# Kernel tuning notes

Hardware: AMD Instinct MI355X
Metric: run time of the kernel (lower is better)

Reference implementation:

```python
import jax, jax.numpy as jnp
import numpy as np
import math

N = 4096
E = 512          # hidden_dim
H = 8            # num_heads
MAX_STEPS = 100
D_TIME = E // 2  # 256
D_STAT = E // 4  # 128


def _time_encoding():
    # sinusoidal table [MAX_STEPS, D_TIME], matching the torch buffer
    pos = jnp.arange(MAX_STEPS, dtype=jnp.float32)[:, None]
    div = jnp.exp(jnp.arange(0, D_TIME, 2, dtype=jnp.float32) * (-math.log(10000.0) / D_TIME))
    ang = pos * div  # [MAX_STEPS, D_TIME//2]
    return jnp.stack([jnp.sin(ang), jnp.cos(ang)], axis=-1).reshape(MAX_STEPS, D_TIME)


def setup_inputs() -> dict:
    key = jax.random.key(0)
    ks = jax.random.split(key, 12)
    w = 0.02
    return {
        "x": jax.random.normal(ks[0], (N, E), jnp.float32),
        "derived_mask": jax.random.randint(ks[1], (N,), 0, 2, jnp.int32),
        "step_numbers": jax.random.randint(ks[2], (N,), 0, MAX_STEPS, jnp.int32),
        "status_embed": jax.random.normal(ks[3], (2, D_STAT), jnp.float32),
        "in_proj_w": jax.random.normal(ks[4], (3 * E, E), jnp.float32) * w,
        "in_proj_b": jnp.zeros((3 * E,), jnp.float32),
        "out_proj_w": jax.random.normal(ks[5], (E, E), jnp.float32) * w,
        "out_proj_b": jnp.zeros((E,), jnp.float32),
        "mlp_w": jax.random.normal(ks[6], (E, E + D_STAT + D_TIME), jnp.float32) * w,
        "mlp_b": jnp.zeros((E,), jnp.float32),
        "ln_gamma": jnp.ones((E,), jnp.float32),
        "ln_beta": jnp.zeros((E,), jnp.float32),
    }


def reference(x, derived_mask, step_numbers, status_embed, in_proj_w, in_proj_b,
              out_proj_w, out_proj_b, mlp_w, mlp_b, ln_gamma, ln_beta):
    n = x.shape[0]
    hd = E // H

    # --- multihead self-attention with dynamic step-based mask ---
    qkv = x @ in_proj_w.T + in_proj_b                      # [N, 3E]
    q, k, v = jnp.split(qkv, 3, axis=-1)
    q = q.reshape(n, H, hd).transpose(1, 0, 2)             # [H, N, hd]
    k = k.reshape(n, H, hd).transpose(1, 0, 2)
    v = v.reshape(n, H, hd).transpose(1, 0, 2)

    scores = jnp.einsum('hnd,hmd->hnm', q, k) / math.sqrt(hd)   # [H, N, N]
    # mask[i, j] = True  <=>  step[j] - step[i] < 0 (blocked, -inf)
    blocked = (step_numbers[None, :] - step_numbers[:, None]) < 0
    scores = jnp.where(blocked[None, :, :], jnp.float32(-1e9), scores)
    attn = jax.nn.softmax(scores, axis=-1)
    ctx = jnp.einsum('hnm,hmd->hnd', attn, v)              # [H, N, hd]
    ctx = ctx.transpose(1, 0, 2).reshape(n, E)
    x_att = ctx @ out_proj_w.T + out_proj_b                # [N, E]

    # --- embeddings ---
    status = status_embed[derived_mask]                    # [N, E/4]
    step_c = jnp.clip(step_numbers, 0, MAX_STEPS - 1)
    time_emb = _time_encoding()[step_c]                    # [N, E/2]

    # --- fused output MLP: Linear -> LayerNorm -> ReLU ---
    combined = jnp.concatenate([x_att, status, time_emb], axis=-1)  # [N, 7E/4]
    h = combined @ mlp_w.T + mlp_b                         # [N, E]
    mu = jnp.mean(h, axis=-1, keepdims=True)
    var = jnp.mean((h - mu) ** 2, axis=-1, keepdims=True)
    h = (h - mu) / jnp.sqrt(var + 1e-5) * ln_gamma + ln_beta
    out = jnp.maximum(h, 0.0)
    return x + out
```

## Files before the change

kernel.cpp:

```cpp
#include <hip/hip_runtime.h>
#include <hip/hip_bf16.h>
#include <math.h>

typedef __bf16 bf16x8 __attribute__((ext_vector_type(8)));
typedef __bf16 bf16x4 __attribute__((ext_vector_type(4)));
typedef float f32x4 __attribute__((ext_vector_type(4)));

#define N_TOK 4096
#define EDIM 512
#define NHEAD 8
#define HD 64
#define LDCOMB 896
#define NBIN 100
#define SPLITK 8
#define BK 64

#define NU_CVT 3264
#define NU_TC 64
#define NU_ADD 128
#define NU_TMAT 128
#define NB_PREP (NU_CVT + NU_TC + NU_ADD + NU_TMAT + 1)

__global__ __launch_bounds__(256) void prep_kernel(
    const float* __restrict__ x, const float* __restrict__ w_in,
    const float* __restrict__ w_mlp, const float* __restrict__ w_out,
    const float* __restrict__ status, const float* __restrict__ out_b,
    const float* __restrict__ mlp_b, const int* __restrict__ steps,
    __bf16* __restrict__ x_bf, __bf16* __restrict__ wqkv_bf,
    __bf16* __restrict__ wmlp_bf, __bf16* __restrict__ woutT_bf,
    float* __restrict__ add2, __bf16* __restrict__ tmat,
    int* __restrict__ perm, int* __restrict__ sstep,
    int* __restrict__ bs_row, int* __restrict__ qinfo) {
    __shared__ float T[64][65];
    __shared__ int hist[NBIN];
    __shared__ int offs[NBIN];
    const int bid = blockIdx.x;
    const int tid = threadIdx.x;
    const int wave = tid >> 6, lane = tid & 63;

    if (bid < NU_CVT) {
        int i = bid * 256 + tid;
        const int n0 = N_TOK * EDIM / 4;
        const int n1 = 3 * EDIM * EDIM / 4;
        const float* src; __bf16* dst;
        if (i < n0)           { src = x; dst = x_bf; }
        else if (i < n0 + n1) { i -= n0; src = w_in; dst = wqkv_bf; }
        else                  { i -= n0 + n1; src = w_mlp; dst = wmlp_bf; }
        const float4 v = ((const float4*)src)[i];
        bf16x4 o;
        o[0] = (__bf16)v.x; o[1] = (__bf16)v.y; o[2] = (__bf16)v.z; o[3] = (__bf16)v.w;
        ((bf16x4*)dst)[i] = o;
    } else if (bid < NU_CVT + NU_TC) {
        const int b2 = bid - NU_CVT;
        const int m0 = (b2 >> 3) * 64, k0 = (b2 & 7) * 64;
        const int row = tid >> 2, c4 = (tid & 3) * 16;
        #pragma unroll
        for (int i = 0; i < 4; i++) {
            const float4 v = *(const float4*)&w_out[(size_t)(m0 + row) * EDIM + k0 + c4 + i * 4];
            T[row][c4 + i * 4 + 0] = v.x;
            T[row][c4 + i * 4 + 1] = v.y;
            T[row][c4 + i * 4 + 2] = v.z;
            T[row][c4 + i * 4 + 3] = v.w;
        }
        __syncthreads();
        const int kr = tid >> 2, m16 = (tid & 3) * 16;
        bf16x8 o0, o1;
        #pragma unroll
        for (int i = 0; i < 8; i++) o0[i] = (__bf16)T[m16 + i][kr];
        #pragma unroll
        for (int i = 0; i < 8; i++) o1[i] = (__bf16)T[m16 + 8 + i][kr];
        *(bf16x8*)&woutT_bf[(size_t)(k0 + kr) * EDIM + m0 + m16] = o0;
        *(bf16x8*)&woutT_bf[(size_t)(k0 + kr) * EDIM + m0 + m16 + 8] = o1;
    } else if (bid < NU_CVT + NU_TC + NU_ADD) {
        const int j = (bid - NU_CVT - NU_TC) * 4 + wave;
        const float* wr = w_mlp + (size_t)j * LDCOMB;
        const int k8 = lane * 8;
        const float4 wa = *(const float4*)&wr[k8], wb = *(const float4*)&wr[k8 + 4];
        const float4 oa = *(const float4*)&out_b[k8], ob = *(const float4*)&out_b[k8 + 4];
        float b = wa.x * oa.x + wa.y * oa.y + wa.z * oa.z + wa.w * oa.w +
                  wb.x * ob.x + wb.y * ob.y + wb.z * ob.z + wb.w * ob.w;
        const int c2 = lane * 2;
        const float w0 = wr[EDIM + c2], w1 = wr[EDIM + c2 + 1];
        float s0 = status[c2] * w0 + status[c2 + 1] * w1;
        float s1 = status[128 + c2] * w0 + status[129 + c2] * w1;
        #pragma unroll
        for (int m = 1; m < 64; m <<= 1) {
            b += __shfl_xor(b, m);
            s0 += __shfl_xor(s0, m);
            s1 += __shfl_xor(s1, m);
        }
        if (lane == 0) {
            const float bb = b + mlp_b[j];
            add2[j] = s0 + bb;
            add2[EDIM + j] = s1 + bb;
        }
    } else if (bid < NU_CVT + NU_TC + NU_ADD + NU_TMAT) {
        const int st = bid - NU_CVT - NU_TC - NU_ADD;
        const int c = tid;
        const int pp = c >> 1;
        const float div = expf((float)(2 * pp) * (-9.210340371976184f / 256.0f));
        const float ang = (float)st * div;
        tmat[st * 256 + c] = (__bf16)((c & 1) ? cosf(ang) : sinf(ang));
    } else {
        if (tid < NBIN) hist[tid] = 0;
        __syncthreads();
        for (int i = tid; i < N_TOK; i += 256)
            atomicAdd(&hist[min(max(steps[i], 0), NBIN - 1)], 1);
        __syncthreads();
        if (tid == 0) {
            int acc = 0;
            for (int s = 0; s < NBIN; s++) { offs[s] = acc; acc += hist[s]; }
        }
        __syncthreads();
        if (tid < NBIN) hist[tid] = offs[tid];
        __syncthreads();
        for (int i = tid; i < N_TOK; i += 256) {
            const int s = min(max(steps[i], 0), NBIN - 1);
            const int pos = atomicAdd(&offs[s], 1);
            perm[pos] = i;
            sstep[pos] = s;
        }
        __syncthreads();
        for (int q = tid; q < N_TOK; q += 256)
            bs_row[q] = hist[sstep[q]];
        __syncthreads();
        for (int qt = tid; qt < 64; qt += 256) {
            qinfo[qt * 2] = bs_row[qt * 64] & ~(BK - 1);
            qinfo[qt * 2 + 1] = bs_row[qt * 64 + 63];
        }
    }
}

__global__ __launch_bounds__(256) void gemm2_kernel(const __bf16* __restrict__ x_bf,
                                                    const __bf16* __restrict__ wqkv_bf,
                                                    const float* __restrict__ b_in,
                                                    const int* __restrict__ perm,
                                                    __bf16* __restrict__ qs,
                                                    __bf16* __restrict__ ks,
                                                    __bf16* __restrict__ vt,
                                                    const __bf16* __restrict__ wmlp_bf,
                                                    const __bf16* __restrict__ woutT_bf,
                                                    __bf16* __restrict__ weff_bf,
                                                    const __bf16* __restrict__ tmat,
                                                    float* __restrict__ tv) {
    __shared__ __attribute__((aligned(16))) union {
        struct { __bf16 As[128][40]; __bf16 Bs[128][40]; } g;
        __bf16 T[128][72];
    } sm;
    __shared__ int pr[128];
    const int bid = blockIdx.x;
    const int tid = threadIdx.x;
    const int wave = tid >> 6, lane = tid & 63;
    const int wm = (wave >> 1) * 64, wn = (wave & 1) * 64;
    const int lr = lane & 15, lq = lane >> 4;

    const __bf16 *A, *B;
    int lda, ldb, bm, bn, K, mode;
    if (bid < 384) {
        A = x_bf; lda = EDIM; B = wqkv_bf; ldb = EDIM; K = EDIM; mode = 0;
        bm = (bid & 31) * 128; bn = (bid >> 5) * 128;
        if (tid < 128) pr[tid] = perm[bm + tid];
    } else if (bid < 400) {
        const int b2 = bid - 384;
        A = wmlp_bf; lda = LDCOMB; B = woutT_bf; ldb = EDIM; K = EDIM; mode = 1;
        bm = (b2 & 3) * 128; bn = (b2 >> 2) * 128;
    } else {
        const int b3 = bid - 400;
        A = tmat; lda = 256; B = wmlp_bf + 640; ldb = LDCOMB; K = 256; mode = 2;
        bm = 0; bn = b3 * 128;
    }

    f32x4 acc[4][4] = {};
    for (int k0 = 0; k0 < K; k0 += 32) {
        __syncthreads();
        #pragma unroll
        for (int c = tid; c < 512; c += 256) {
            const int row = c >> 2, k8 = (c & 3) * 8;
            const int arow = (mode == 0) ? pr[row] : (bm + row);
            *(bf16x8*)&sm.g.As[row][k8] = *(const bf16x8*)&A[(size_t)arow * lda + k0 + k8];
            *(bf16x8*)&sm.g.Bs[row][k8] = *(const bf16x8*)&B[(size_t)(bn + row) * ldb + k0 + k8];
        }
        __syncthreads();
        bf16x8 af[4], bfr[4];
        #pragma unroll
        for (int i = 0; i < 4; i++) {
            af[i]  = *(const bf16x8*)&sm.g.As[wm + i * 16 + lr][lq * 8];
            bfr[i] = *(const bf16x8*)&sm.g.Bs[wn + i * 16 + lr][lq * 8];
        }
        #pragma unroll
        for (int i = 0; i < 4; i++)
            #pragma unroll
            for (int j = 0; j < 4; j++)
                acc[i][j] = __builtin_amdgcn_mfma_f32_16x16x32_bf16(af[i], bfr[j], acc[i][j], 0, 0, 0);
    }

    if (mode == 1) {
        #pragma unroll
        for (int i = 0; i < 4; i++)
            #pragma unroll
            for (int j = 0; j < 4; j++) {
                const int col = bn + wn + j * 16 + lr;
                #pragma unroll
                for (int r = 0; r < 4; r++)
                    weff_bf[(size_t)(bm + wm + i * 16 + lq * 4 + r) * EDIM + col] =
                        (__bf16)acc[i][j][r];
            }
    } else if (mode == 2) {
        #pragma unroll
        for (int i = 0; i < 4; i++)
            #pragma unroll
            for (int j = 0; j < 4; j++) {
                const int col = bn + wn + j * 16 + lr;
                #pragma unroll
                for (int r = 0; r < 4; r++) {
                    const int row = wm + i * 16 + lq * 4 + r;
                    if (row < NBIN) tv[(size_t)row * EDIM + col] = acc[i][j][r];
                }
            }
    } else if (bn < 512) {
        const float SC = 0.125f * 1.44269504f;
        #pragma unroll
        for (int i = 0; i < 4; i++)
            #pragma unroll
            for (int j = 0; j < 4; j++) {
                const int col = bn + wn + j * 16 + lr;
                const float bv = b_in[col];
                #pragma unroll
                for (int r = 0; r < 4; r++)
                    qs[(size_t)(bm + wm + i * 16 + lq * 4 + r) * EDIM + col] =
                        (__bf16)((acc[i][j][r] + bv) * SC);
            }
    } else if (bn < 1024) {
        #pragma unroll
        for (int i = 0; i < 4; i++)
            #pragma unroll
            for (int j = 0; j < 4; j++) {
                const int col = bn + wn + j * 16 + lr;
                const float bv = b_in[col];
                #pragma unroll
                for (int r = 0; r < 4; r++)
                    ks[(size_t)(bm + wm + i * 16 + lq * 4 + r) * EDIM + (col - 512)] =
                        (__bf16)(acc[i][j][r] + bv);
            }
    } else {
        #pragma unroll
        for (int half = 0; half < 2; half++) {
            __syncthreads();
            if ((wave & 1) == half) {
                #pragma unroll
                for (int i = 0; i < 4; i++)
                    #pragma unroll
                    for (int j = 0; j < 4; j++) {
                        const float bv = b_in[bn + wn + j * 16 + lr];
                        #pragma unroll
                        for (int r = 0; r < 4; r++)
                            sm.T[wm + i * 16 + lq * 4 + r][j * 16 + lr] =
                                (__bf16)(acc[i][j][r] + bv);
                    }
            }
            __syncthreads();
            for (int u = tid; u < 1024; u += 256) {
                const int d = u & 63, t8 = (u >> 6) * 8;
                bf16x8 v;
                #pragma unroll
                for (int j = 0; j < 8; j++) v[j] = sm.T[t8 + j][d];
                const int dim = (bn - 1024) + half * 64 + d;
                *(bf16x8*)&vt[(size_t)dim * N_TOK + bm + t8] = v;
            }
        }
    }
}

__global__ __launch_bounds__(256) void attn_kernel(const __bf16* __restrict__ qs,
                                                   const __bf16* __restrict__ ks,
                                                   const __bf16* __restrict__ vt,
                                                   const int* __restrict__ bs_row,
                                                   const int* __restrict__ qinfo,
                                                   __bf16* __restrict__ po,
                                                   float* __restrict__ pl) {
    __shared__ __attribute__((aligned(16))) __bf16 Ks[BK][72];
    __shared__ __attribute__((aligned(16))) __bf16 Vs[64][BK + 8];
    __shared__ __attribute__((aligned(16))) __bf16 Ps[64][BK + 8];

    const int h = blockIdx.y;
    const int qtile = blockIdx.x;
    const int ck = blockIdx.z;
    const int tid = threadIdx.x, wave = tid >> 6, lane = tid & 63;
    const int lr = lane & 15, lq = lane >> 4;
    const int qbase = qtile * 64 + wave * 16;

    const int kt0 = qinfo[qtile * 2];
    const int bs_blockmax = qinfo[qtile * 2 + 1];
    const int nt = (N_TOK - kt0) / BK;
    const int kta = kt0 + ((nt * ck) / SPLITK) * BK;
    const int ktb = kt0 + ((nt * (ck + 1)) / SPLITK) * BK;

    bf16x8 aq[2];
    {
        const __bf16* qrow = qs + (size_t)(qbase + lr) * EDIM + h * HD;
        aq[0] = *(const bf16x8*)&qrow[lq * 8];
        aq[1] = *(const bf16x8*)&qrow[32 + lq * 8];
    }
    int bs_r[4];
    #pragma unroll
    for (int r = 0; r < 4; r++) bs_r[r] = bs_row[qbase + lq * 4 + r];

    float l_i[4] = {0.f, 0.f, 0.f, 0.f};
    f32x4 o[4] = {};

    const __bf16* kbase = ks + h * HD;
    const __bf16* vbase = vt + (size_t)h * HD * N_TOK;

    const int r0 = tid >> 3, r1 = r0 + 32, k8 = (tid & 7) * 8;
    bf16x8 kr0, kr1, vr0, vr1;
    if (kta < ktb) {
        kr0 = *(const bf16x8*)&kbase[(size_t)(kta + r0) * EDIM + k8];
        kr1 = *(const bf16x8*)&kbase[(size_t)(kta + r1) * EDIM + k8];
        vr0 = *(const bf16x8*)&vbase[(size_t)r0 * N_TOK + kta + k8];
        vr1 = *(const bf16x8*)&vbase[(size_t)r1 * N_TOK + kta + k8];
    }

    for (int kt = kta; kt < ktb; kt += BK) {
        __syncthreads();
        *(bf16x8*)&Ks[r0][k8] = kr0;
        *(bf16x8*)&Ks[r1][k8] = kr1;
        *(bf16x8*)&Vs[r0][k8] = vr0;
        *(bf16x8*)&Vs[r1][k8] = vr1;
        __syncthreads();
        if (kt + BK < ktb) {
            kr0 = *(const bf16x8*)&kbase[(size_t)(kt + BK + r0) * EDIM + k8];
            kr1 = *(const bf16x8*)&kbase[(size_t)(kt + BK + r1) * EDIM + k8];
            vr0 = *(const bf16x8*)&vbase[(size_t)r0 * N_TOK + kt + BK + k8];
            vr1 = *(const bf16x8*)&vbase[(size_t)r1 * N_TOK + kt + BK + k8];
        }

        f32x4 s[4];
        #pragma unroll
        for (int t = 0; t < 4; t++) {
            bf16x8 b0 = *(const bf16x8*)&Ks[t * 16 + lr][lq * 8];
            bf16x8 b1 = *(const bf16x8*)&Ks[t * 16 + lr][32 + lq * 8];
            f32x4 a = {};
            a = __builtin_amdgcn_mfma_f32_16x16x32_bf16(aq[0], b0, a, 0, 0, 0);
            a = __builtin_amdgcn_mfma_f32_16x16x32_bf16(aq[1], b1, a, 0, 0, 0);
            s[t] = a;
        }
        if (kt < bs_blockmax) {
            #pragma unroll
            for (int t = 0; t < 4; t++) {
                const int col = kt + t * 16 + lr;
                #pragma unroll
                for (int r = 0; r < 4; r++)
                    if (col < bs_r[r]) s[t][r] = -1e9f;
            }
        }
        #pragma unroll
        for (int t = 0; t < 4; t++) {
            #pragma unroll
            for (int r = 0; r < 4; r++) {
                const float pr = exp2f(s[t][r]);
                l_i[r] += pr;
                Ps[wave * 16 + lq * 4 + r][t * 16 + lr] = (__bf16)pr;
            }
        }
        #pragma unroll
        for (int ks2 = 0; ks2 < 2; ks2++) {
            bf16x8 ap = *(const bf16x8*)&Ps[wave * 16 + lr][ks2 * 32 + lq * 8];
            #pragma unroll
            for (int dt = 0; dt < 4; dt++) {
                bf16x8 bv = *(const bf16x8*)&Vs[dt * 16 + lr][ks2 * 32 + lq * 8];
                o[dt] = __builtin_amdgcn_mfma_f32_16x16x32_bf16(ap, bv, o[dt], 0, 0, 0);
            }
        }
    }

    #pragma unroll
    for (int r = 0; r < 4; r++) {
        float v = l_i[r];
        v += __shfl_xor(v, 1);
        v += __shfl_xor(v, 2);
        v += __shfl_xor(v, 4);
        v += __shfl_xor(v, 8);
        l_i[r] = v;
    }
    __bf16* pob = po + (((size_t)(ck * NHEAD + h) * N_TOK) + qbase) * HD;
    #pragma unroll
    for (int dt = 0; dt < 4; dt++)
        #pragma unroll
        for (int r = 0; r < 4; r++)
            pob[(lq * 4 + r) * HD + dt * 16 + lr] = (__bf16)o[dt][r];
    if (lr == 0) {
        #pragma unroll
        for (int r = 0; r < 4; r++)
            pl[(size_t)(ck * NHEAD + h) * N_TOK + qbase + lq * 4 + r] = l_i[r];
    }
}

__global__ __launch_bounds__(256) void combine_kernel(const __bf16* __restrict__ po,
                                                      const float* __restrict__ pl,
                                                      const int* __restrict__ perm,
                                                      __bf16* __restrict__ ctx) {
    const int e = blockIdx.x * 256 + threadIdx.x;
    const int q = e >> 7;
    const int col = (e & 127) * 4;
    const int h = col >> 6, d = col & 63;
    float s0 = 0.f, s1 = 0.f, s2 = 0.f, s3 = 0.f, l = 0.f;
    #pragma unroll
    for (int c = 0; c < SPLITK; c++) {
        const bf16x4 v = *(const bf16x4*)&po[(((size_t)(c * NHEAD + h) * N_TOK) + q) * HD + d];
        s0 += (float)v[0]; s1 += (float)v[1]; s2 += (float)v[2]; s3 += (float)v[3];
        l += pl[(size_t)(c * NHEAD + h) * N_TOK + q];
    }
    const float rl = 1.0f / l;
    bf16x4 o;
    o[0] = (__bf16)(s0 * rl); o[1] = (__bf16)(s1 * rl);
    o[2] = (__bf16)(s2 * rl); o[3] = (__bf16)(s3 * rl);
    *(bf16x4*)&ctx[(size_t)perm[q] * EDIM + col] = o;
}

__global__ __launch_bounds__(256) void gemm_fused(const __bf16* __restrict__ A,
                                                  const __bf16* __restrict__ B,
                                                  const int* __restrict__ dmask,
                                                  const int* __restrict__ steps,
                                                  const float* __restrict__ add2,
                                                  const float* __restrict__ tv,
                                                  float* __restrict__ C) {
    __shared__ __attribute__((aligned(16))) __bf16 As[128][40];
    __shared__ __attribute__((aligned(16))) __bf16 Bs[128][40];
    const int tid = threadIdx.x;
    const int wave = tid >> 6, lane = tid & 63;
    const int wm = (wave >> 1) * 64, wn = (wave & 1) * 64;
    const int bm = blockIdx.x * 128, bn = blockIdx.y * 128;
    const int lr = lane & 15, lq = lane >> 4;

    f32x4 acc[4][4] = {};
    for (int k0 = 0; k0 < EDIM; k0 += 32) {
        __syncthreads();
        #pragma unroll
        for (int c = tid; c < 512; c += 256) {
            const int row = c >> 2, k8 = (c & 3) * 8;
            *(bf16x8*)&As[row][k8] = *(const bf16x8*)&A[(size_t)(bm + row) * EDIM + k0 + k8];
            *(bf16x8*)&Bs[row][k8] = *(const bf16x8*)&B[(size_t)(bn + row) * EDIM + k0 + k8];
        }
        __syncthreads();
        bf16x8 af[4], bfr[4];
        #pragma unroll
        for (int i = 0; i < 4; i++) {
            af[i]  = *(const bf16x8*)&As[wm + i * 16 + lr][lq * 8];
            bfr[i] = *(const bf16x8*)&Bs[wn + i * 16 + lr][lq * 8];
        }
        #pragma unroll
        for (int i = 0; i < 4; i++)
            #pragma unroll
            for (int j = 0; j < 4; j++)
                acc[i][j] = __builtin_amdgcn_mfma_f32_16x16x32_bf16(af[i], bfr[j], acc[i][j], 0, 0, 0);
    }

    int dmr[4][4], str[4][4];
    #pragma unroll
    for (int i = 0; i < 4; i++)
        #pragma unroll
        for (int r = 0; r < 4; r++) {
            const int row = bm + wm + i * 16 + lq * 4 + r;
            dmr[i][r] = dmask[row];
            str[i][r] = min(max(steps[row], 0), NBIN - 1);
        }
    #pragma unroll
    for (int i = 0; i < 4; i++)
        #pragma unroll
        for (int j = 0; j < 4; j++) {
            const int col = bn + wn + j * 16 + lr;
            #pragma unroll
            for (int r = 0; r < 4; r++) {
                const int row = bm + wm + i * 16 + lq * 4 + r;
                C[(size_t)row * EDIM + col] = acc[i][j][r]
                    + add2[dmr[i][r] * EDIM + col] + tv[str[i][r] * EDIM + col];
            }
        }
}

__global__ __launch_bounds__(256) void ln_kernel(const float* __restrict__ h,
                                                 const float* __restrict__ x,
                                                 const float* __restrict__ gamma,
                                                 const float* __restrict__ beta,
                                                 float* __restrict__ out) {
    const int row = blockIdx.x * 4 + (threadIdx.x >> 6);
    const int lane = threadIdx.x & 63;
    const float* hr = h + (size_t)row * EDIM;
    float4 v0 = ((const float4*)hr)[lane];
    float4 v1 = ((const float4*)hr)[64 + lane];
    float sum = v0.x + v0.y + v0.z + v0.w + v1.x + v1.y + v1.z + v1.w;
    float sq = v0.x * v0.x + v0.y * v0.y + v0.z * v0.z + v0.w * v0.w +
               v1.x * v1.x + v1.y * v1.y + v1.z * v1.z + v1.w * v1.w;
    #pragma unroll
    for (int m = 1; m < 64; m <<= 1) {
        sum += __shfl_xor(sum, m);
        sq  += __shfl_xor(sq, m);
    }
    const float mean = sum * (1.0f / EDIM);
    const float var = sq * (1.0f / EDIM) - mean * mean;
    const float rstd = rsqrtf(var + 1e-5f);
    const float* xr = x + (size_t)row * EDIM;
    float* orow = out + (size_t)row * EDIM;
    #pragma unroll
    for (int half = 0; half < 2; half++) {
        const float4 v = half ? v1 : v0;
        const int cb = half * 256 + lane * 4;
        const float* vp = (const float*)&v;
        float4 res;
        float tmp[4];
        #pragma unroll
        for (int i = 0; i < 4; i++) {
            const int c = cb + i;
            float t = (vp[i] - mean) * rstd * gamma[c] + beta[c];
            t = fmaxf(t, 0.f);
            tmp[i] = xr[c] + t;
        }
        res.x = tmp[0]; res.y = tmp[1]; res.z = tmp[2]; res.w = tmp[3];
        ((float4*)orow)[cb >> 2] = res;
    }
}

extern "C" void kernel_launch(void* const* d_in, const int* in_sizes, int n_in,
                              void* d_out, int out_size, void* d_ws, size_t ws_size,
                              hipStream_t stream) {
    const float* x      = (const float*)d_in[0];
    const int*   dmask  = (const int*)d_in[1];
    const int*   steps  = (const int*)d_in[2];
    const float* status = (const float*)d_in[3];
    const float* w_in   = (const float*)d_in[4];
    const float* b_in   = (const float*)d_in[5];
    const float* w_out  = (const float*)d_in[6];
    const float* b_out  = (const float*)d_in[7];
    const float* w_mlp  = (const float*)d_in[8];
    const float* b_mlp  = (const float*)d_in[9];
    const float* gamma  = (const float*)d_in[10];
    const float* beta   = (const float*)d_in[11];
    float* out = (float*)d_out;

    char* ws = (char*)d_ws;
    size_t off = 0;
    auto alloc = [&](size_t bytes) {
        void* ptr = ws + off;
        off = (off + bytes + 255) & ~(size_t)255;
        return ptr;
    };
    __bf16* x_bf    = (__bf16*)alloc((size_t)N_TOK * EDIM * 2);
    __bf16* wqkv_bf = (__bf16*)alloc((size_t)3 * EDIM * EDIM * 2);
    __bf16* wmlp_bf = (__bf16*)alloc((size_t)EDIM * LDCOMB * 2);
    __bf16* woutT_bf= (__bf16*)alloc((size_t)EDIM * EDIM * 2);
    __bf16* weff_bf = (__bf16*)alloc((size_t)EDIM * EDIM * 2);
    __bf16* qs_bf   = (__bf16*)alloc((size_t)N_TOK * EDIM * 2);
    __bf16* ks_bf   = (__bf16*)alloc((size_t)N_TOK * EDIM * 2);
    __bf16* vt_bf   = (__bf16*)alloc((size_t)EDIM * N_TOK * 2);
    __bf16* ctx_bf  = (__bf16*)alloc((size_t)N_TOK * EDIM * 2);
    float*  h_f32   = (float*)alloc((size_t)N_TOK * EDIM * 4);
    int*    perm    = (int*)alloc(N_TOK * 4);
    int*    sstep   = (int*)alloc(N_TOK * 4);
    int*    bs_row  = (int*)alloc(N_TOK * 4);
    int*    qinfo   = (int*)alloc(128 * 4);
    __bf16* po      = (__bf16*)alloc((size_t)SPLITK * NHEAD * N_TOK * HD * 2);
    float*  pl      = (float*)alloc((size_t)SPLITK * NHEAD * N_TOK * 4);
    float*  add2    = (float*)alloc(2 * EDIM * 4);
    float*  tv      = (float*)alloc((size_t)NBIN * EDIM * 4);
    __bf16* tmat    = (__bf16*)alloc(128 * 256 * 2);

    prep_kernel<<<NB_PREP, 256, 0, stream>>>(
        x, w_in, w_mlp, w_out, status, b_out, b_mlp, steps,
        x_bf, wqkv_bf, wmlp_bf, woutT_bf, add2, tmat, perm, sstep, bs_row, qinfo);
    gemm2_kernel<<<404, 256, 0, stream>>>(
        x_bf, wqkv_bf, b_in, perm, qs_bf, ks_bf, vt_bf,
        wmlp_bf, woutT_bf, weff_bf, tmat, tv);
    attn_kernel<<<dim3(64, NHEAD, SPLITK), 256, 0, stream>>>(
        qs_bf, ks_bf, vt_bf, bs_row, qinfo, po, pl);
    combine_kernel<<<(N_TOK * EDIM) / 1024, 256, 0, stream>>>(po, pl, perm, ctx_bf);
    gemm_fused<<<dim3(N_TOK / 128, EDIM / 128), 256, 0, stream>>>(
        ctx_bf, weff_bf, dmask, steps, add2, tv, h_f32);
    ln_kernel<<<N_TOK / 4, 256, 0, stream>>>(h_f32, x, gamma, beta, out);
}
```

Baseline: 204.2 us.

## Fuse fp32-to-bf16 conversion into GEMM tile loads and narrow final GEMM tiles

Drops the separate conversion pass over x, w_in and w_mlp from the prep kernel. The QKV and weight GEMMs now read fp32 directly and convert to bf16 while loading tiles into shared memory, which removes a full write-and-reread of the bf16 copies. In exchange those GEMM loads fetch twice as many bytes per element and take a runtime branch on the source type. Separately, the final fused GEMM switches from 128x128 to 128x64 tiles, doubling the block count to 256 so more of the GPU is occupied, at the cost of reloading A tiles more often.

```diff
diff --git a/kernel.cpp b/kernel.cpp
--- a/kernel.cpp
+++ b/kernel.cpp
@@ -15,19 +15,25 @@
 #define SPLITK 8
 #define BK 64
 
-#define NU_CVT 3264
 #define NU_TC 64
 #define NU_ADD 128
 #define NU_TMAT 128
-#define NB_PREP (NU_CVT + NU_TC + NU_ADD + NU_TMAT + 1)
+#define NB_PREP (NU_TC + NU_ADD + NU_TMAT + 1)
+
+__device__ __forceinline__ bf16x8 cvt8(const float* p) {
+    const float4 a = *(const float4*)p;
+    const float4 b = *(const float4*)(p + 4);
+    bf16x8 o;
+    o[0] = (__bf16)a.x; o[1] = (__bf16)a.y; o[2] = (__bf16)a.z; o[3] = (__bf16)a.w;
+    o[4] = (__bf16)b.x; o[5] = (__bf16)b.y; o[6] = (__bf16)b.z; o[7] = (__bf16)b.w;
+    return o;
+}
 
 __global__ __launch_bounds__(256) void prep_kernel(
-    const float* __restrict__ x, const float* __restrict__ w_in,
     const float* __restrict__ w_mlp, const float* __restrict__ w_out,
     const float* __restrict__ status, const float* __restrict__ out_b,
     const float* __restrict__ mlp_b, const int* __restrict__ steps,
-    __bf16* __restrict__ x_bf, __bf16* __restrict__ wqkv_bf,
-    __bf16* __restrict__ wmlp_bf, __bf16* __restrict__ woutT_bf,
+    __bf16* __restrict__ woutT_bf,
     float* __restrict__ add2, __bf16* __restrict__ tmat,
     int* __restrict__ perm, int* __restrict__ sstep,
     int* __restrict__ bs_row, int* __restrict__ qinfo) {
@@ -38,21 +44,8 @@
     const int tid = threadIdx.x;
     const int wave = tid >> 6, lane = tid & 63;
 
-    if (bid < NU_CVT) {
-        int i = bid * 256 + tid;
-        const int n0 = N_TOK * EDIM / 4;
-        const int n1 = 3 * EDIM * EDIM / 4;
-        const float* src; __bf16* dst;
-        if (i < n0)           { src = x; dst = x_bf; }
-        else if (i < n0 + n1) { i -= n0; src = w_in; dst = wqkv_bf; }
-        else                  { i -= n0 + n1; src = w_mlp; dst = wmlp_bf; }
-        const float4 v = ((const float4*)src)[i];
-        bf16x4 o;
-        o[0] = (__bf16)v.x; o[1] = (__bf16)v.y; o[2] = (__bf16)v.z; o[3] = (__bf16)v.w;
-        ((bf16x4*)dst)[i] = o;
-    } else if (bid < NU_CVT + NU_TC) {
-        const int b2 = bid - NU_CVT;
-        const int m0 = (b2 >> 3) * 64, k0 = (b2 & 7) * 64;
+    if (bid < NU_TC) {
+        const int m0 = (bid >> 3) * 64, k0 = (bid & 7) * 64;
         const int row = tid >> 2, c4 = (tid & 3) * 16;
         #pragma unroll
         for (int i = 0; i < 4; i++) {
@@ -71,8 +64,8 @@
         for (int i = 0; i < 8; i++) o1[i] = (__bf16)T[m16 + 8 + i][kr];
         *(bf16x8*)&woutT_bf[(size_t)(k0 + kr) * EDIM + m0 + m16] = o0;
         *(bf16x8*)&woutT_bf[(size_t)(k0 + kr) * EDIM + m0 + m16 + 8] = o1;
-    } else if (bid < NU_CVT + NU_TC + NU_ADD) {
-        const int j = (bid - NU_CVT - NU_TC) * 4 + wave;
+    } else if (bid < NU_TC + NU_ADD) {
+        const int j = (bid - NU_TC) * 4 + wave;
         const float* wr = w_mlp + (size_t)j * LDCOMB;
         const int k8 = lane * 8;
         const float4 wa = *(const float4*)&wr[k8], wb = *(const float4*)&wr[k8 + 4];
@@ -94,8 +87,8 @@
             add2[j] = s0 + bb;
             add2[EDIM + j] = s1 + bb;
         }
-    } else if (bid < NU_CVT + NU_TC + NU_ADD + NU_TMAT) {
-        const int st = bid - NU_CVT - NU_TC - NU_ADD;
+    } else if (bid < NU_TC + NU_ADD + NU_TMAT) {
+        const int st = bid - NU_TC - NU_ADD;
         const int c = tid;
         const int pp = c >> 1;
         const float div = expf((float)(2 * pp) * (-9.210340371976184f / 256.0f));
@@ -131,14 +124,14 @@
     }
 }
 
-__global__ __launch_bounds__(256) void gemm2_kernel(const __bf16* __restrict__ x_bf,
-                                                    const __bf16* __restrict__ wqkv_bf,
+__global__ __launch_bounds__(256) void gemm2_kernel(const float* __restrict__ x,
+                                                    const float* __restrict__ w_in,
                                                     const float* __restrict__ b_in,
                                                     const int* __restrict__ perm,
                                                     __bf16* __restrict__ qs,
                                                     __bf16* __restrict__ ks,
                                                     __bf16* __restrict__ vt,
-                                                    const __bf16* __restrict__ wmlp_bf,
+                                                    const float* __restrict__ w_mlp,
                                                     const __bf16* __restrict__ woutT_bf,
                                                     __bf16* __restrict__ weff_bf,
                                                     const __bf16* __restrict__ tmat,
@@ -154,19 +147,20 @@
     const int wm = (wave >> 1) * 64, wn = (wave & 1) * 64;
     const int lr = lane & 15, lq = lane >> 4;
 
-    const __bf16 *A, *B;
+    const float *Af = nullptr, *Bf = nullptr;
+    const __bf16 *Ab = nullptr, *Bb = nullptr;
     int lda, ldb, bm, bn, K, mode;
     if (bid < 384) {
-        A = x_bf; lda = EDIM; B = wqkv_bf; ldb = EDIM; K = EDIM; mode = 0;
+        Af = x; lda = EDIM; Bf = w_in; ldb = EDIM; K = EDIM; mode = 0;
         bm = (bid & 31) * 128; bn = (bid >> 5) * 128;
         if (tid < 128) pr[tid] = perm[bm + tid];
     } else if (bid < 400) {
         const int b2 = bid - 384;
-        A = wmlp_bf; lda = LDCOMB; B = woutT_bf; ldb = EDIM; K = EDIM; mode = 1;
+        Af = w_mlp; lda = LDCOMB; Bb = woutT_bf; ldb = EDIM; K = EDIM; mode = 1;
         bm = (b2 & 3) * 128; bn = (b2 >> 2) * 128;
     } else {
         const int b3 = bid - 400;
-        A = tmat; lda = 256; B = wmlp_bf + 640; ldb = LDCOMB; K = 256; mode = 2;
+        Ab = tmat; lda = 256; Bf = w_mlp + 640; ldb = LDCOMB; K = 256; mode = 2;
         bm = 0; bn = b3 * 128;
     }
 
@@ -177,8 +171,13 @@
         for (int c = tid; c < 512; c += 256) {
             const int row = c >> 2, k8 = (c & 3) * 8;
             const int arow = (mode == 0) ? pr[row] : (bm + row);
-            *(bf16x8*)&sm.g.As[row][k8] = *(const bf16x8*)&A[(size_t)arow * lda + k0 + k8];
-            *(bf16x8*)&sm.g.Bs[row][k8] = *(const bf16x8*)&B[(size_t)(bn + row) * ldb + k0 + k8];
+            bf16x8 av, bv;
+            if (Af) av = cvt8(&Af[(size_t)arow * lda + k0 + k8]);
+            else    av = *(const bf16x8*)&Ab[(size_t)arow * lda + k0 + k8];
+            if (Bf) bv = cvt8(&Bf[(size_t)(bn + row) * ldb + k0 + k8]);
+            else    bv = *(const bf16x8*)&Bb[(size_t)(bn + row) * ldb + k0 + k8];
+            *(bf16x8*)&sm.g.As[row][k8] = av;
+            *(bf16x8*)&sm.g.Bs[row][k8] = bv;
         }
         __syncthreads();
         bf16x8 af[4], bfr[4];
@@ -425,39 +424,45 @@
                                                   const float* __restrict__ tv,
                                                   float* __restrict__ C) {
     __shared__ __attribute__((aligned(16))) __bf16 As[128][40];
-    __shared__ __attribute__((aligned(16))) __bf16 Bs[128][40];
+    __shared__ __attribute__((aligned(16))) __bf16 Bs[64][40];
     const int tid = threadIdx.x;
     const int wave = tid >> 6, lane = tid & 63;
-    const int wm = (wave >> 1) * 64, wn = (wave & 1) * 64;
-    const int bm = blockIdx.x * 128, bn = blockIdx.y * 128;
+    const int wm = wave * 32;
+    const int bm = blockIdx.x * 128, bn = blockIdx.y * 64;
     const int lr = lane & 15, lq = lane >> 4;
 
-    f32x4 acc[4][4] = {};
+    f32x4 acc[2][4] = {};
     for (int k0 = 0; k0 < EDIM; k0 += 32) {
         __syncthreads();
         #pragma unroll
-        for (int c = tid; c < 512; c += 256) {
-            const int row = c >> 2, k8 = (c & 3) * 8;
-            *(bf16x8*)&As[row][k8] = *(const bf16x8*)&A[(size_t)(bm + row) * EDIM + k0 + k8];
-            *(bf16x8*)&Bs[row][k8] = *(const bf16x8*)&B[(size_t)(bn + row) * EDIM + k0 + k8];
-        }
-        __syncthreads();
-        bf16x8 af[4], bfr[4];
-        #pragma unroll
-        for (int i = 0; i < 4; i++) {
-            af[i]  = *(const bf16x8*)&As[wm + i * 16 + lr][lq * 8];
-            bfr[i] = *(const bf16x8*)&Bs[wn + i * 16 + lr][lq * 8];
-        }
-        #pragma unroll
-        for (int i = 0; i < 4; i++)
+        for (int c = tid; c < 768; c += 256) {
+            if (c < 512) {
+                const int row = c >> 2, k8 = (c & 3) * 8;
+                *(bf16x8*)&As[row][k8] = *(const bf16x8*)&A[(size_t)(bm + row) * EDIM + k0 + k8];
+            } else {
+                const int c2 = c - 512;
+                const int row = c2 >> 2, k8 = (c2 & 3) * 8;
+                *(bf16x8*)&Bs[row][k8] = *(const bf16x8*)&B[(size_t)(bn + row) * EDIM + k0 + k8];
+            }
+        }
+        __syncthreads();
+        bf16x8 af[2], bfr[4];
+        #pragma unroll
+        for (int i = 0; i < 2; i++)
+            af[i] = *(const bf16x8*)&As[wm + i * 16 + lr][lq * 8];
+        #pragma unroll
+        for (int j = 0; j < 4; j++)
+            bfr[j] = *(const bf16x8*)&Bs[j * 16 + lr][lq * 8];
+        #pragma unroll
+        for (int i = 0; i < 2; i++)
             #pragma unroll
             for (int j = 0; j < 4; j++)
                 acc[i][j] = __builtin_amdgcn_mfma_f32_16x16x32_bf16(af[i], bfr[j], acc[i][j], 0, 0, 0);
     }
 
-    int dmr[4][4], str[4][4];
-    #pragma unroll
-    for (int i = 0; i < 4; i++)
+    int dmr[2][4], str[2][4];
+    #pragma unroll
+    for (int i = 0; i < 2; i++)
         #pragma unroll
         for (int r = 0; r < 4; r++) {
             const int row = bm + wm + i * 16 + lq * 4 + r;
@@ -465,10 +470,10 @@
             str[i][r] = min(max(steps[row], 0), NBIN - 1);
         }
     #pragma unroll
-    for (int i = 0; i < 4; i++)
+    for (int i = 0; i < 2; i++)
         #pragma unroll
         for (int j = 0; j < 4; j++) {
-            const int col = bn + wn + j * 16 + lr;
+            const int col = bn + j * 16 + lr;
             #pragma unroll
             for (int r = 0; r < 4; r++) {
                 const int row = bm + wm + i * 16 + lq * 4 + r;
@@ -544,9 +549,6 @@
         off = (off + bytes + 255) & ~(size_t)255;
         return ptr;
     };
-    __bf16* x_bf    = (__bf16*)alloc((size_t)N_TOK * EDIM * 2);
-    __bf16* wqkv_bf = (__bf16*)alloc((size_t)3 * EDIM * EDIM * 2);
-    __bf16* wmlp_bf = (__bf16*)alloc((size_t)EDIM * LDCOMB * 2);
     __bf16* woutT_bf= (__bf16*)alloc((size_t)EDIM * EDIM * 2);
     __bf16* weff_bf = (__bf16*)alloc((size_t)EDIM * EDIM * 2);
     __bf16* qs_bf   = (__bf16*)alloc((size_t)N_TOK * EDIM * 2);
@@ -565,15 +567,15 @@
     __bf16* tmat    = (__bf16*)alloc(128 * 256 * 2);
 
     prep_kernel<<<NB_PREP, 256, 0, stream>>>(
-        x, w_in, w_mlp, w_out, status, b_out, b_mlp, steps,
-        x_bf, wqkv_bf, wmlp_bf, woutT_bf, add2, tmat, perm, sstep, bs_row, qinfo);
+        w_mlp, w_out, status, b_out, b_mlp, steps,
+        woutT_bf, add2, tmat, perm, sstep, bs_row, qinfo);
     gemm2_kernel<<<404, 256, 0, stream>>>(
-        x_bf, wqkv_bf, b_in, perm, qs_bf, ks_bf, vt_bf,
-        wmlp_bf, woutT_bf, weff_bf, tmat, tv);
+        x, w_in, b_in, perm, qs_bf, ks_bf, vt_bf,
+        w_mlp, woutT_bf, weff_bf, tmat, tv);
     attn_kernel<<<dim3(64, NHEAD, SPLITK), 256, 0, stream>>>(
         qs_bf, ks_bf, vt_bf, bs_row, qinfo, po, pl);
     combine_kernel<<<(N_TOK * EDIM) / 1024, 256, 0, stream>>>(po, pl, perm, ctx_bf);
-    gemm_fused<<<dim3(N_TOK / 128, EDIM / 128), 256, 0, stream>>>(
+    gemm_fused<<<dim3(N_TOK / 128, EDIM / 64), 256, 0, stream>>>(
         ctx_bf, weff_bf, dmask, steps, add2, tv, h_f32);
     ln_kernel<<<N_TOK / 4, 256, 0, stream>>>(h_f32, x, gamma, beta, out);
 }
```

Result: slower. 216.2 us (+5.9%).
